# Kernel tuning notes

Measured on AMD Instinct MI355X. Metric: run time of the kernel, lower is better.

The kernel has to match this reference:

```python
import jax, jax.numpy as jnp
import numpy as np

N = 4096
E = 131072
IN_C, HID, HEADS, OUT_C = 512, 64, 8, 256
BETA = 0.5
NEG_SLOPE = 0.2


def _glorot(key, shape, fan_in, fan_out):
    lim = float(np.sqrt(6.0 / (fan_in + fan_out)))
    return jax.random.uniform(key, shape, jnp.float32, -lim, lim)


def setup_inputs() -> dict:
    key = jax.random.key(0)
    ks = jax.random.split(key, 12)
    x = jax.random.normal(ks[0], (N, IN_C), jnp.float32)
    src = jax.random.randint(ks[1], (E,), 0, N)
    dst = jax.random.randint(ks[2], (E,), 0, N)
    dst = jnp.where(src == dst, (dst + 1) % N, dst)  # no self loops (module removes then re-adds)
    edge_index = jnp.stack([src, dst]).astype(jnp.int64)
    # layer 1: in=512 -> heads=8, out=64 (concat -> 512), residual=False
    W1 = _glorot(ks[3], (IN_C, HEADS * HID), IN_C, HEADS * HID)
    as1 = _glorot(ks[4], (HEADS, HID), HID, HID)
    ad1 = _glorot(ks[5], (HEADS, HID), HID, HID)
    b1 = jnp.zeros((HEADS * HID,), jnp.float32)
    # layer 2: in=512 -> heads=1, out=256, concat=False, residual=True (res_linear needed)
    W2 = _glorot(ks[6], (HEADS * HID, OUT_C), HEADS * HID, OUT_C)
    as2 = _glorot(ks[7], (1, OUT_C), OUT_C, OUT_C)
    ad2 = _glorot(ks[8], (1, OUT_C), OUT_C, OUT_C)
    b2 = jnp.zeros((OUT_C,), jnp.float32)
    resW2 = _glorot(ks[9], (HEADS * HID, OUT_C), HEADS * HID, OUT_C)
    return {"x": x, "edge_index": edge_index, "W1": W1, "as1": as1, "ad1": ad1,
            "b1": b1, "W2": W2, "as2": as2, "ad2": ad2, "b2": b2, "resW2": resW2}


def _seg_softmax(e, seg, n):
    # numerically-stable softmax over edges grouped by destination node
    m = jax.ops.segment_max(e, seg, num_segments=n)  # [n, H]
    a = jnp.exp(e - m[seg])
    s = jax.ops.segment_sum(a, seg, num_segments=n)
    return a / (s[seg] + 1e-16)


def _motif_gat_layer(x, edge_index, W, a_src, a_dst, bias, res_W, heads, out_ch, concat):
    n = x.shape[0]
    residual = x
    h = (x @ W).reshape(n, heads, out_ch)
    # add self loops (input edge_index has none)
    loops = jnp.arange(n, dtype=edge_index.dtype)
    src = jnp.concatenate([edge_index[0], loops])
    dst = jnp.concatenate([edge_index[1], loops])
    xj = h[src]  # [E', H, C]
    xi = h[dst]
    e = (xj * a_src[None]).sum(-1) + (xi * a_dst[None]).sum(-1)  # [E', H]
    alpha_first = _seg_softmax(jax.nn.leaky_relu(e, NEG_SLOPE), dst, n)
    # motif adjacency: dense A^3, row-normalized by clamped row sum
    adj = jnp.zeros((n, n), x.dtype).at[src, dst].set(1.0)
    m3 = adj @ adj @ adj
    m3 = m3 / jnp.clip(m3.sum(-1, keepdims=True), 1.0)
    mw = m3[src, dst][:, None]  # [E', 1]
    alpha_motif = _seg_softmax(jax.nn.leaky_relu(e * mw, NEG_SLOPE), dst, n)
    alpha = BETA * alpha_first + (1.0 - BETA) * alpha_motif  # dropout: eval mode -> identity
    out = jax.ops.segment_sum(alpha[:, :, None] * xj, dst, num_segments=n)  # [n, H, C]
    out = out.reshape(n, heads * out_ch) if concat else out.mean(1)
    if res_W is not None:
        out = out + residual @ res_W
    return out + bias


def reference(x, edge_index, W1, as1, ad1, b1, W2, as2, ad2, b2, resW2):
    h = _motif_gat_layer(x, edge_index, W1, as1, ad1, b1, None, HEADS, HID, True)
    h = jax.nn.elu(h)  # dropout: eval mode -> identity
    out = _motif_gat_layer(h, edge_index, W2, as2, ad2, b2, resW2, 1, OUT_C, False)
    return out
```

## Files before the change

kernel.cpp:

```cpp
#include <hip/hip_runtime.h>
#include <hip/hip_bf16.h>
#include <math.h>

#define NN 4096
#define EE 131072
#define EP (EE + NN)
#define C1 512
#define H1 8
#define C2 256
#define NWORDS 128
#define KP 520

typedef __attribute__((ext_vector_type(8))) short bf16x8;
typedef __attribute__((ext_vector_type(4))) float f32x4;

__device__ __forceinline__ float wredMaxf(float v){
#pragma unroll
  for(int o=32;o;o>>=1) v = fmaxf(v, __shfl_xor(v,o));
  return v;
}
__device__ __forceinline__ float wredSumf(float v){
#pragma unroll
  for(int o=32;o;o>>=1) v += __shfl_xor(v,o);
  return v;
}
__device__ __forceinline__ int wredSumi(int v){
#pragma unroll
  for(int o=32;o;o>>=1) v += __shfl_xor(v,o);
  return v;
}

__device__ __forceinline__ void bfsplit(float v, unsigned short& h, unsigned short& l){
  unsigned bits = __float_as_uint(v);
  h = (unsigned short)(bits>>16);
  float hf = __uint_as_float(bits & 0xFFFF0000u);
  float lo = v - hf;
  l = (unsigned short)(__float_as_uint(lo)>>16);
}

__device__ __forceinline__ int detect_mode(const int* __restrict__ ei32){
  unsigned nz = 0;
#pragma unroll
  for(int i=1;i<16;i+=2) nz |= (unsigned)ei32[i];
  return nz != 0;
}

__device__ __forceinline__ void edge_sd(const int* ei32, int mode, int e, int& s, int& d){
  if(e < EE){
    if(mode==0){ s = ei32[2*e]; d = ei32[2*(EE+e)]; }
    else       { s = ei32[e];   d = ei32[EE+e]; }
  } else { s = e - EE; d = s; }
}

__global__ __launch_bounds__(256) void k_build(const int* __restrict__ ei32,
    unsigned* __restrict__ rowbits, unsigned* __restrict__ colbits, unsigned* __restrict__ cnt){
  int e = blockIdx.x*256 + threadIdx.x;
  if(e >= EP) return;
  int m = detect_mode(ei32), s, d;
  edge_sd(ei32, m, e, s, d);
  atomicOr(&rowbits[s*NWORDS + (d>>5)], 1u<<(d&31));
  atomicOr(&colbits[d*NWORDS + (s>>5)], 1u<<(s&31));
  atomicAdd(&cnt[d], 1u);
}

__global__ __launch_bounds__(256) void k_scan_deg(const unsigned* __restrict__ cnt, unsigned* __restrict__ rowptr,
    const unsigned* __restrict__ rowbits, float* __restrict__ v1){
  int t = threadIdx.x;
  if(blockIdx.x == 0){
    __shared__ unsigned part[256];
    unsigned loc[16]; unsigned s = 0;
#pragma unroll
    for(int i=0;i<16;i++){ loc[i]=cnt[t*16+i]; s+=loc[i]; }
    part[t]=s; __syncthreads();
    for(int off=1;off<256;off<<=1){
      unsigned v = (t>=off)? part[t-off] : 0u;
      __syncthreads();
      part[t]+=v;
      __syncthreads();
    }
    unsigned run = (t==0)? 0u : part[t-1];
#pragma unroll
    for(int i=0;i<16;i++){ rowptr[t*16+i]=run; run+=loc[i]; }
    if(t==255) rowptr[NN]=run;
  } else {
    int node = (blockIdx.x-1)*4 + (t>>6);
    int lane = t & 63;
    unsigned w0 = rowbits[node*NWORDS + 2*lane];
    unsigned w1 = rowbits[node*NWORDS + 2*lane + 1];
    int c = __popc(w0) + __popc(w1);
    c = wredSumi(c);
    if(lane==0) v1[node] = (float)c;
  }
}

__global__ __launch_bounds__(256) void k_fill_mv(const int* __restrict__ ei32,
    const unsigned* __restrict__ rowptr, unsigned* __restrict__ fill, unsigned* __restrict__ csr_src,
    const unsigned* __restrict__ rowbits, const float* __restrict__ v1, float* __restrict__ v2){
  int t = threadIdx.x;
  if(blockIdx.x < 528){
    int e = blockIdx.x*256 + t;
    if(e >= EP) return;
    int m = detect_mode(ei32), s, d;
    edge_sd(ei32, m, e, s, d);
    unsigned pos = rowptr[d] + atomicAdd(&fill[d], 1u);
    csr_src[pos]=(unsigned)s;
  } else {
    int node = (blockIdx.x-528)*4 + (t>>6);
    int lane = t & 63;
    float sum = 0.f;
    unsigned w = rowbits[node*NWORDS + 2*lane]; int b0 = lane*64;
    while(w){ int b=__ffs(w)-1; sum += v1[b0+b]; w &= w-1; }
    w = rowbits[node*NWORDS + 2*lane + 1]; b0 = lane*64 + 32;
    while(w){ int b=__ffs(w)-1; sum += v1[b0+b]; w &= w-1; }
    sum = wredSumf(sum);
    if(lane==0) v2[node] = sum;
  }
}

__global__ __launch_bounds__(256) void k_mv2_cvt(const unsigned* __restrict__ rowbits,
    const float* __restrict__ v2, float* __restrict__ v3,
    const float* __restrict__ X, unsigned short* __restrict__ xh, unsigned short* __restrict__ xl,
    const float* __restrict__ W1f, const float* __restrict__ W2f, const float* __restrict__ Wrf,
    unsigned short* __restrict__ b1h, unsigned short* __restrict__ b1l,
    unsigned short* __restrict__ b2h, unsigned short* __restrict__ b2l){
  int t = threadIdx.x;
  int b = blockIdx.x;
  if(b < 1024){
    int node = b*4 + (t>>6);
    int lane = t & 63;
    float sum = 0.f;
    unsigned w = rowbits[node*NWORDS + 2*lane]; int b0 = lane*64;
    while(w){ int bb=__ffs(w)-1; sum += v2[b0+bb]; w &= w-1; }
    w = rowbits[node*NWORDS + 2*lane + 1]; b0 = lane*64 + 32;
    while(w){ int bb=__ffs(w)-1; sum += v2[b0+bb]; w &= w-1; }
    sum = wredSumf(sum);
    if(lane==0) v3[node] = sum;
  } else if(b < 2048){
    int e = (b-1024)*256 + t;
    int row = e >> 6;
    int c0 = (e & 63) * 8;
    const float4 v0 = *(const float4*)&X[(size_t)row*C1 + c0];
    const float4 v1q = *(const float4*)&X[(size_t)row*C1 + c0 + 4];
    float vv[8] = {v0.x,v0.y,v0.z,v0.w,v1q.x,v1q.y,v1q.z,v1q.w};
    unsigned short h[8], l[8];
#pragma unroll
    for(int j=0;j<8;j++) bfsplit(vv[j], h[j], l[j]);
    *(bf16x8*)&xh[(size_t)row*KP + c0] = *(bf16x8*)h;
    *(bf16x8*)&xl[(size_t)row*KP + c0] = *(bf16x8*)l;
  } else {
    int blk = b - 2048;
    const float* W; int N, n, nrow; unsigned short *bh, *bl;
    if(blk < 512){ W=W1f; N=512; n=blk;     nrow=n;     bh=b1h; bl=b1l; }
    else if(blk < 768){ W=W2f; N=256; n=blk-512; nrow=n;     bh=b2h; bl=b2l; }
    else { W=Wrf; N=256; n=blk-768; nrow=n+256; bh=b2h; bl=b2l; }
    int k = t*2;
    float a = W[(size_t)k*N + n];
    float bb = W[(size_t)(k+1)*N + n];
    unsigned short h0,l0,h1,l1;
    bfsplit(a,h0,l0); bfsplit(bb,h1,l1);
    unsigned short hp[2]={h0,h1}, lp[2]={l0,l1};
    *(unsigned int*)&bh[(size_t)nrow*KP + k] = *(unsigned int*)hp;
    *(unsigned int*)&bl[(size_t)nrow*KP + k] = *(unsigned int*)lp;
  }
}

__global__ __launch_bounds__(64) void k_motif(const unsigned* __restrict__ rowbits, const unsigned* __restrict__ colbits,
    const unsigned* __restrict__ rowptr, const unsigned* __restrict__ csr_src,
    const float* __restrict__ v3, float* __restrict__ mwc){
  int d = blockIdx.x;
  int lane = threadIdx.x;
  __shared__ unsigned short nbr[1024];
  __shared__ int cntL;
  if(lane==0) cntL=0;
  __syncthreads();
  {
    unsigned w = colbits[d*NWORDS + 2*lane]; int b0 = lane*64;
    while(w){ int b=__ffs(w)-1; int pos=atomicAdd(&cntL,1); nbr[pos]=(unsigned short)(b0+b); w&=w-1; }
    w = colbits[d*NWORDS + 2*lane + 1]; b0 = lane*64 + 32;
    while(w){ int b=__ffs(w)-1; int pos=atomicAdd(&cntL,1); nbr[pos]=(unsigned short)(b0+b); w&=w-1; }
  }
  __syncthreads();
  int m = cntL;
  unsigned gp[8][2];
#pragma unroll
  for(int p=0;p<8;p++){ gp[p][0]=0u; gp[p][1]=0u; }
  for(int t0=0;t0<m;t0+=4){
    unsigned xa[4], xb[4];
#pragma unroll
    for(int j=0;j<4;j++){
      int tt=t0+j;
      if(tt<m){ int l = nbr[tt]; xa[j]=colbits[l*NWORDS+2*lane]; xb[j]=colbits[l*NWORDS+2*lane+1]; }
      else    { xa[j]=0u; xb[j]=0u; }
    }
#pragma unroll
    for(int j=0;j<4;j++){
      unsigned c = xa[j];
#pragma unroll
      for(int p=0;p<8;p++){ unsigned cy = gp[p][0] & c; gp[p][0] ^= c; c = cy; }
      c = xb[j];
#pragma unroll
      for(int p=0;p<8;p++){ unsigned cy = gp[p][1] & c; gp[p][1] ^= c; c = cy; }
    }
  }
  unsigned base = rowptr[d], deg = rowptr[d+1]-base;
  for(unsigned i0=0;i0<deg;i0+=4){
    unsigned sidx[4], ra[4], rb[4];
#pragma unroll
    for(int j=0;j<4;j++){
      unsigned ii = (i0+j < deg) ? (i0+j) : (deg-1);
      sidx[j] = csr_src[base+ii];
    }
#pragma unroll
    for(int j=0;j<4;j++){ ra[j]=rowbits[sidx[j]*NWORDS+2*lane]; rb[j]=rowbits[sidx[j]*NWORDS+2*lane+1]; }
    int sum[4];
#pragma unroll
    for(int j=0;j<4;j++){
      int s=0;
#pragma unroll
      for(int p=0;p<8;p++)
        s += (__popc(ra[j]&gp[p][0]) + __popc(rb[j]&gp[p][1])) << p;
      sum[j]=s;
    }
    int pk0 = sum[0] | (sum[1]<<16);
    int pk1 = sum[2] | (sum[3]<<16);
    pk0 = wredSumi(pk0); pk1 = wredSumi(pk1);
    if(lane==0){
      int ss[4] = { pk0 & 0xFFFF, (pk0>>16)&0xFFFF, pk1 & 0xFFFF, (pk1>>16)&0xFFFF };
#pragma unroll
      for(int j=0;j<4;j++){
        unsigned idx = i0+j;
        if(idx<deg)
          mwc[base+idx] = (float)ss[j] / fmaxf(v3[csr_src[base+idx]], 1.0f);
      }
    }
  }
}

__global__ __launch_bounds__(256) void k_gemm_mfma(
    const unsigned short* __restrict__ Ah, const unsigned short* __restrict__ Al,
    const unsigned short* __restrict__ Bh, const unsigned short* __restrict__ Bl,
    float* __restrict__ C, int M, int N,
    const float* __restrict__ aS, const float* __restrict__ aD,
    float* __restrict__ oS, float* __restrict__ oD, int amode){
  __shared__ unsigned short Ahs[64][72], Als[64][72], Bhs[64][72], Bls[64][72];
  int bm = blockIdx.y*64, bn = blockIdx.x*64;
  int t = threadIdx.x, lane = t&63, w = t>>6;
  int wm = (w>>1)*32, wn = (w&1)*32;
  f32x4 acc[2][2];
#pragma unroll
  for(int i=0;i<2;i++)
#pragma unroll
    for(int j=0;j<2;j++) acc[i][j] = (f32x4){0.f,0.f,0.f,0.f};
  int sm = t>>2, sk = (t&3)*16;
  const unsigned short* pAh = &Ah[(size_t)(bm+sm)*KP + sk];
  const unsigned short* pAl = &Al[(size_t)(bm+sm)*KP + sk];
  const unsigned short* pBh = &Bh[(size_t)(bn+sm)*KP + sk];
  const unsigned short* pBl = &Bl[(size_t)(bn+sm)*KP + sk];
  int fr = lane&15, kg = lane>>4;
  bf16x8 rah0 = *(const bf16x8*)(pAh), rah1 = *(const bf16x8*)(pAh+8);
  bf16x8 ral0 = *(const bf16x8*)(pAl), ral1 = *(const bf16x8*)(pAl+8);
  bf16x8 rbh0 = *(const bf16x8*)(pBh), rbh1 = *(const bf16x8*)(pBh+8);
  bf16x8 rbl0 = *(const bf16x8*)(pBl), rbl1 = *(const bf16x8*)(pBl+8);
  *(bf16x8*)&Ahs[sm][sk] = rah0; *(bf16x8*)&Ahs[sm][sk+8] = rah1;
  *(bf16x8*)&Als[sm][sk] = ral0; *(bf16x8*)&Als[sm][sk+8] = ral1;
  *(bf16x8*)&Bhs[sm][sk] = rbh0; *(bf16x8*)&Bhs[sm][sk+8] = rbh1;
  *(bf16x8*)&Bls[sm][sk] = rbl0; *(bf16x8*)&Bls[sm][sk+8] = rbl1;
  __syncthreads();
  for(int k0=0;k0<C1;k0+=64){
    int kn = k0+64;
    if(kn<C1){
      rah0 = *(const bf16x8*)(pAh+kn); rah1 = *(const bf16x8*)(pAh+kn+8);
      ral0 = *(const bf16x8*)(pAl+kn); ral1 = *(const bf16x8*)(pAl+kn+8);
      rbh0 = *(const bf16x8*)(pBh+kn); rbh1 = *(const bf16x8*)(pBh+kn+8);
      rbl0 = *(const bf16x8*)(pBl+kn); rbl1 = *(const bf16x8*)(pBl+kn+8);
    }
#pragma unroll
    for(int ks=0;ks<64;ks+=32){
      bf16x8 fah[2], fal[2], fbh[2], fbl[2];
#pragma unroll
      for(int i=0;i<2;i++){
        fah[i] = *(bf16x8*)&Ahs[wm + i*16 + fr][ks + kg*8];
        fal[i] = *(bf16x8*)&Als[wm + i*16 + fr][ks + kg*8];
        fbh[i] = *(bf16x8*)&Bhs[wn + i*16 + fr][ks + kg*8];
        fbl[i] = *(bf16x8*)&Bls[wn + i*16 + fr][ks + kg*8];
      }
#pragma unroll
      for(int i=0;i<2;i++)
#pragma unroll
        for(int j=0;j<2;j++){
          acc[i][j] = __builtin_amdgcn_mfma_f32_16x16x32_bf16(fah[i], fbh[j], acc[i][j], 0,0,0);
          acc[i][j] = __builtin_amdgcn_mfma_f32_16x16x32_bf16(fah[i], fbl[j], acc[i][j], 0,0,0);
          acc[i][j] = __builtin_amdgcn_mfma_f32_16x16x32_bf16(fal[i], fbh[j], acc[i][j], 0,0,0);
        }
    }
    __syncthreads();
    if(kn<C1){
      *(bf16x8*)&Ahs[sm][sk] = rah0; *(bf16x8*)&Ahs[sm][sk+8] = rah1;
      *(bf16x8*)&Als[sm][sk] = ral0; *(bf16x8*)&Als[sm][sk+8] = ral1;
      *(bf16x8*)&Bhs[sm][sk] = rbh0; *(bf16x8*)&Bhs[sm][sk+8] = rbh1;
      *(bf16x8*)&Bls[sm][sk] = rbl0; *(bf16x8*)&Bls[sm][sk+8] = rbl1;
    }
    __syncthreads();
  }
#pragma unroll
  for(int i=0;i<2;i++)
#pragma unroll
    for(int j=0;j<2;j++){
      int gr = bm + wm + i*16 + kg*4;
      int gc = bn + wn + j*16 + fr;
#pragma unroll
      for(int e=0;e<4;e++)
        C[(size_t)(gr+e)*N + gc] = acc[i][j][e];
    }
  bool do_attn = (amode==1) || (bn < 256);
  if(do_attn){
    float p1[2][4], p2[2][4];
#pragma unroll
    for(int i=0;i<2;i++)
#pragma unroll
      for(int e=0;e<4;e++){ p1[i][e]=0.f; p2[i][e]=0.f; }
#pragma unroll
    for(int j=0;j<2;j++){
      int col = bn + wn + j*16 + fr;
      float a1c = aS[col], a2c = aD[col];
#pragma unroll
      for(int i=0;i<2;i++)
#pragma unroll
        for(int e=0;e<4;e++){ p1[i][e] += acc[i][j][e]*a1c; p2[i][e] += acc[i][j][e]*a2c; }
    }
#pragma unroll
    for(int o=1;o<16;o<<=1){
#pragma unroll
      for(int i=0;i<2;i++)
#pragma unroll
        for(int e=0;e<4;e++){ p1[i][e]+=__shfl_xor(p1[i][e],o); p2[i][e]+=__shfl_xor(p2[i][e],o); }
    }
    if(fr==0){
      int head = (amode==1)? (bn>>6) : 0;
      int hs = (amode==1)? H1 : 1;
#pragma unroll
      for(int i=0;i<2;i++)
#pragma unroll
        for(int e=0;e<4;e++){
          int row = bm + wm + i*16 + kg*4 + e;
          atomicAdd(&oS[row*hs + head], p1[i][e]);
          atomicAdd(&oD[row*hs + head], p2[i][e]);
        }
    }
  }
}

__global__ __launch_bounds__(128) void k_layer1(const unsigned* __restrict__ rowptr, const unsigned* __restrict__ csr_src,
    const float* __restrict__ mwc, const float* __restrict__ asrc, const float* __restrict__ adst,
    const float* __restrict__ hpre, const float* __restrict__ b1,
    unsigned short* __restrict__ h1h, unsigned short* __restrict__ h1l){
  int n = blockIdx.x;
  int tid = threadIdx.x, lane = tid&63, wv = tid>>6;
  unsigned base = rowptr[n], deg = rowptr[n+1]-base;
  __shared__ float a1s[128][9];
  __shared__ float a2s[128][9];
  __shared__ unsigned ssrc[128];
  __shared__ float red1[2][8], red2[2][8];
  __shared__ float snm1[8], snm2[8], sscl1[8], sscl2[8];
  __shared__ float sS1[8], sS2[8], sM1[8], sM2[8];
  __shared__ float adsts[8];
  if(tid<8){ adsts[tid]=adst[n*H1+tid]; sM1[tid]=-3.0e38f; sM2[tid]=-3.0e38f; sS1[tid]=0.f; sS2[tid]=0.f; }
  __syncthreads();
  int h = tid>>4;
  float4 acc1={0.f,0.f,0.f,0.f}, acc2={0.f,0.f,0.f,0.f};
  for(unsigned c0=0;c0<deg;c0+=128){
    int csz = (int)min(128u, deg-c0);
    bool act = (tid < csz);
    float el[8], em[8];
    if(act){
      unsigned s = csr_src[base+c0+tid];
      ssrc[tid]=s;
      float mwv = mwc[base+c0+tid];
      const float4 a0v = *(const float4*)&asrc[s*H1];
      const float4 a1v = *(const float4*)&asrc[s*H1+4];
      float as8[8]={a0v.x,a0v.y,a0v.z,a0v.w,a1v.x,a1v.y,a1v.z,a1v.w};
#pragma unroll
      for(int hh=0;hh<8;hh++){
        float ev = as8[hh]+adsts[hh];
        el[hh] = ev>=0.f? ev : 0.2f*ev;
        float evm = ev*mwv;
        em[hh] = evm>=0.f? evm : 0.2f*evm;
      }
    } else {
#pragma unroll
      for(int hh=0;hh<8;hh++){ el[hh]=-3.0e38f; em[hh]=-3.0e38f; }
    }
    float mx1[8], mx2[8];
#pragma unroll
    for(int hh=0;hh<8;hh++){ mx1[hh]=wredMaxf(el[hh]); mx2[hh]=wredMaxf(em[hh]); }
    if(lane==0){
#pragma unroll
      for(int hh=0;hh<8;hh++){ red1[wv][hh]=mx1[hh]; red2[wv][hh]=mx2[hh]; }
    }
    __syncthreads();
    if(tid<8){
      float cm1 = fmaxf(red1[0][tid], red1[1][tid]);
      float cm2 = fmaxf(red2[0][tid], red2[1][tid]);
      float nm1 = fmaxf(sM1[tid], cm1), nm2 = fmaxf(sM2[tid], cm2);
      sscl1[tid] = expf(sM1[tid]-nm1); sscl2[tid] = expf(sM2[tid]-nm2);
      snm1[tid]=nm1; snm2[tid]=nm2;
      sM1[tid]=nm1;  sM2[tid]=nm2;
    }
    __syncthreads();
    float s1l[8], s2l[8];
#pragma unroll
    for(int hh=0;hh<8;hh++){
      float a1v = act? expf(el[hh]-snm1[hh]) : 0.f;
      float a2v = act? expf(em[hh]-snm2[hh]) : 0.f;
      if(act){ a1s[tid][hh]=a1v; a2s[tid][hh]=a2v; }
      s1l[hh]=a1v; s2l[hh]=a2v;
    }
#pragma unroll
    for(int hh=0;hh<8;hh++){ s1l[hh]=wredSumf(s1l[hh]); s2l[hh]=wredSumf(s2l[hh]); }
    if(lane==0){
#pragma unroll
      for(int hh=0;hh<8;hh++){ red1[wv][hh]=s1l[hh]; red2[wv][hh]=s2l[hh]; }
    }
    __syncthreads();
    if(tid<8){
      sS1[tid] = sS1[tid]*sscl1[tid] + red1[0][tid]+red1[1][tid];
      sS2[tid] = sS2[tid]*sscl2[tid] + red2[0][tid]+red2[1][tid];
    }
    {
      float sc1 = sscl1[h], sc2 = sscl2[h];
      acc1.x*=sc1; acc1.y*=sc1; acc1.z*=sc1; acc1.w*=sc1;
      acc2.x*=sc2; acc2.y*=sc2; acc2.z*=sc2; acc2.w*=sc2;
    }
    for(int i0=0;i0<csz;i0+=8){
      int jn = min(8, csz-i0);
      unsigned sj[8]; float a1j[8], a2j[8];
#pragma unroll
      for(int j=0;j<8;j++){
        int ii = (j<jn)? i0+j : i0;
        sj[j]=ssrc[ii]; a1j[j]=a1s[ii][h]; a2j[j]=a2s[ii][h];
      }
      float4 hv[8];
#pragma unroll
      for(int j=0;j<8;j++) hv[j] = *(const float4*)&hpre[(size_t)sj[j]*C1 + tid*4];
#pragma unroll
      for(int j=0;j<8;j++){
        float w1 = (j<jn)? a1j[j] : 0.f;
        float w2 = (j<jn)? a2j[j] : 0.f;
        acc1.x += w1*hv[j].x; acc1.y += w1*hv[j].y; acc1.z += w1*hv[j].z; acc1.w += w1*hv[j].w;
        acc2.x += w2*hv[j].x; acc2.y += w2*hv[j].y; acc2.z += w2*hv[j].z; acc2.w += w2*hv[j].w;
      }
    }
    __syncthreads();
  }
  float r1 = 0.5f/(sS1[h]+1e-16f), r2 = 0.5f/(sS2[h]+1e-16f);
  int cc = tid*4;
  const float4 bv = *(const float4*)&b1[cc];
  float o[4];
  float vx = acc1.x*r1 + acc2.x*r2 + bv.x; o[0] = vx>0.f? vx : expm1f(vx);
  float vy = acc1.y*r1 + acc2.y*r2 + bv.y; o[1] = vy>0.f? vy : expm1f(vy);
  float vz = acc1.z*r1 + acc2.z*r2 + bv.z; o[2] = vz>0.f? vz : expm1f(vz);
  float vw = acc1.w*r1 + acc2.w*r2 + bv.w; o[3] = vw>0.f? vw : expm1f(vw);
  unsigned short hh4[4], ll4[4];
#pragma unroll
  for(int j=0;j<4;j++) bfsplit(o[j], hh4[j], ll4[j]);
  *(ushort4*)&h1h[(size_t)n*KP + cc] = *(ushort4*)hh4;
  *(ushort4*)&h1l[(size_t)n*KP + cc] = *(ushort4*)ll4;
}

__global__ __launch_bounds__(64) void k_layer2(const unsigned* __restrict__ rowptr, const unsigned* __restrict__ csr_src,
    const float* __restrict__ mwc, const float* __restrict__ asrc, const float* __restrict__ adst,
    const float* __restrict__ h2, const float* __restrict__ res,
    const float* __restrict__ b2, float* __restrict__ out){
  int n = blockIdx.x; int lane = threadIdx.x;
  unsigned base = rowptr[n], deg = rowptr[n+1]-base;
  __shared__ float a1s[64], a2s[64];
  __shared__ unsigned ssrc[64];
  float ad = adst[n];
  float M1=-3.0e38f, M2=-3.0e38f, S1=0.f, S2=0.f;
  float4 acc1={0.f,0.f,0.f,0.f}, acc2={0.f,0.f,0.f,0.f};
  for(unsigned c0=0;c0<deg;c0+=64){
    int csz = (int)min(64u, deg-c0);
    bool act = (lane < csz);
    float el=-3.0e38f, em=-3.0e38f;
    if(act){
      unsigned s = csr_src[base+c0+lane];
      ssrc[lane]=s;
      float mwv = mwc[base+c0+lane];
      float ev = asrc[s] + ad;
      el = ev>=0.f? ev : 0.2f*ev;
      float evm = ev*mwv;
      em = evm>=0.f? evm : 0.2f*evm;
    }
    float nm1 = fmaxf(M1, wredMaxf(el));
    float nm2 = fmaxf(M2, wredMaxf(em));
    float sc1 = expf(M1-nm1), sc2 = expf(M2-nm2);
    M1=nm1; M2=nm2;
    float a1 = act? expf(el-nm1) : 0.f;
    float a2 = act? expf(em-nm2) : 0.f;
    if(act){ a1s[lane]=a1; a2s[lane]=a2; }
    S1 = S1*sc1 + wredSumf(a1);
    S2 = S2*sc2 + wredSumf(a2);
    acc1.x*=sc1; acc1.y*=sc1; acc1.z*=sc1; acc1.w*=sc1;
    acc2.x*=sc2; acc2.y*=sc2; acc2.z*=sc2; acc2.w*=sc2;
    __syncthreads();
    for(int i0=0;i0<csz;i0+=8){
      int jn = min(8, csz-i0);
      unsigned sj[8]; float a1j[8], a2j[8];
#pragma unroll
      for(int j=0;j<8;j++){
        int ii = (j<jn)? i0+j : i0;
        sj[j]=ssrc[ii]; a1j[j]=a1s[ii]; a2j[j]=a2s[ii];
      }
      float4 hv[8];
#pragma unroll
      for(int j=0;j<8;j++) hv[j] = *(const float4*)&h2[(size_t)sj[j]*512 + lane*4];
#pragma unroll
      for(int j=0;j<8;j++){
        float w1 = (j<jn)? a1j[j] : 0.f;
        float w2 = (j<jn)? a2j[j] : 0.f;
        acc1.x += w1*hv[j].x; acc1.y += w1*hv[j].y; acc1.z += w1*hv[j].z; acc1.w += w1*hv[j].w;
        acc2.x += w2*hv[j].x; acc2.y += w2*hv[j].y; acc2.z += w2*hv[j].z; acc2.w += w2*hv[j].w;
      }
    }
    __syncthreads();
  }
  float r1 = 0.5f/(S1+1e-16f), r2 = 0.5f/(S2+1e-16f);
  int cc = lane*4;
  const float4 rv = *(const float4*)&res[(size_t)n*512 + cc];
  const float4 bv = *(const float4*)&b2[cc];
  float4 o = {acc1.x*r1 + acc2.x*r2 + rv.x + bv.x,
              acc1.y*r1 + acc2.y*r2 + rv.y + bv.y,
              acc1.z*r1 + acc2.z*r2 + rv.z + bv.z,
              acc1.w*r1 + acc2.w*r2 + rv.w + bv.w};
  *(float4*)&out[(size_t)n*C2 + cc] = o;
}

extern "C" void kernel_launch(void* const* d_in, const int* in_sizes, int n_in,
                              void* d_out, int out_size, void* d_ws, size_t ws_size,
                              hipStream_t stream) {
  const float* x    = (const float*)d_in[0];
  const int*   ei32 = (const int*)d_in[1];
  const float* W1   = (const float*)d_in[2];
  const float* as1  = (const float*)d_in[3];
  const float* ad1  = (const float*)d_in[4];
  const float* b1   = (const float*)d_in[5];
  const float* W2   = (const float*)d_in[6];
  const float* as2  = (const float*)d_in[7];
  const float* ad2  = (const float*)d_in[8];
  const float* b2   = (const float*)d_in[9];
  const float* resW2= (const float*)d_in[10];
  float* out = (float*)d_out;

  char* p = (char*)d_ws;
  auto alloc = [&](size_t b){ void* r=(void*)p; p += (b + 255) & ~(size_t)255; return r; };
  unsigned* rowbits = (unsigned*)alloc((size_t)NN*NWORDS*4);
  unsigned* colbits = (unsigned*)alloc((size_t)NN*NWORDS*4);
  unsigned* cnt     = (unsigned*)alloc(NN*4);
  unsigned* fill    = (unsigned*)alloc(NN*4);
  float* asrc1= (float*)alloc(NN*H1*4);
  float* adst1= (float*)alloc(NN*H1*4);
  float* asrc2= (float*)alloc(NN*4);
  float* adst2= (float*)alloc(NN*4);
  size_t zbytes = (size_t)(p - (char*)rowbits);
  unsigned* rowptr  = (unsigned*)alloc((NN+4)*4);
  float* v1 = (float*)alloc(NN*4);
  float* v2 = (float*)alloc(NN*4);
  float* v3 = (float*)alloc(NN*4);
  unsigned* csr_src = (unsigned*)alloc((size_t)EP*4);
  float* mwc  = (float*)alloc((size_t)EP*4);
  unsigned short* xsh = (unsigned short*)alloc((size_t)NN*KP*2);
  unsigned short* xsl = (unsigned short*)alloc((size_t)NN*KP*2);
  unsigned short* bt1h= (unsigned short*)alloc((size_t)C1*KP*2);
  unsigned short* bt1l= (unsigned short*)alloc((size_t)C1*KP*2);
  unsigned short* bt2h= (unsigned short*)alloc((size_t)C1*KP*2);
  unsigned short* bt2l= (unsigned short*)alloc((size_t)C1*KP*2);
  float* hpre = (float*)alloc((size_t)NN*C1*4);
  unsigned short* h1h = (unsigned short*)alloc((size_t)NN*KP*2);
  unsigned short* h1l = (unsigned short*)alloc((size_t)NN*KP*2);
  float* c23  = (float*)alloc((size_t)NN*512*4);
  float* h2  = c23;
  float* res = c23 + 256;

  hipMemsetAsync(rowbits, 0, zbytes, stream);

  k_build<<<(EP+255)/256,256,0,stream>>>(ei32, rowbits, colbits, cnt);
  k_scan_deg<<<1+NN/4,256,0,stream>>>(cnt, rowptr, rowbits, v1);
  k_fill_mv<<<528+NN/4,256,0,stream>>>(ei32, rowptr, fill, csr_src, rowbits, v1, v2);
  k_mv2_cvt<<<3072,256,0,stream>>>(rowbits, v2, v3, x, xsh, xsl, W1, W2, resW2, bt1h, bt1l, bt2h, bt2l);
  k_motif<<<NN,64,0,stream>>>(rowbits, colbits, rowptr, csr_src, v3, mwc);

  k_gemm_mfma<<<dim3(C1/64, NN/64),256,0,stream>>>(xsh, xsl, bt1h, bt1l, hpre, NN, C1,
                                                   as1, ad1, asrc1, adst1, 1);
  k_layer1<<<NN,128,0,stream>>>(rowptr, csr_src, mwc, asrc1, adst1, hpre, b1, h1h, h1l);

  k_gemm_mfma<<<dim3(512/64, NN/64),256,0,stream>>>(h1h, h1l, bt2h, bt2l, c23, NN, 512,
                                                    as2, ad2, asrc2, adst2, 2);
  k_layer2<<<NN,64,0,stream>>>(rowptr, csr_src, mwc, asrc2, adst2, h2, res, b2, out);
}
```

Baseline: 250.9 us.

## Fuse layer-1 GEMM with motif counting, split 4-wave motif, store layer-2 features as bf16

Moves the x/weight bf16 split conversion into the edge-build kernel so it overlaps with graph construction. Merges the layer-1 GEMM and the motif-weight kernel into one launch, with a shared-memory union, so the two independent workloads run concurrently. The motif computation now uses four waves per node and combines their bit-sliced counters through shared memory. The layer-2 GEMM writes the gathered h2 features as round-to-nearest bf16 to halve gather traffic in layer2, which adds rounding error to the aggregated output.

```diff
diff --git a/kernel.cpp b/kernel.cpp
--- a/kernel.cpp
+++ b/kernel.cpp
@@ -38,6 +38,11 @@
   l = (unsigned short)(__float_as_uint(lo)>>16);
 }
 
+__device__ __forceinline__ unsigned short f2bf_rne(float v){
+  unsigned b = __float_as_uint(v);
+  return (unsigned short)((b + 0x7FFFu + ((b>>16)&1u)) >> 16);
+}
+
 __device__ __forceinline__ int detect_mode(const int* __restrict__ ei32){
   unsigned nz = 0;
 #pragma unroll
@@ -52,15 +57,48 @@
   } else { s = e - EE; d = s; }
 }
 
-__global__ __launch_bounds__(256) void k_build(const int* __restrict__ ei32,
-    unsigned* __restrict__ rowbits, unsigned* __restrict__ colbits, unsigned* __restrict__ cnt){
-  int e = blockIdx.x*256 + threadIdx.x;
-  if(e >= EP) return;
-  int m = detect_mode(ei32), s, d;
-  edge_sd(ei32, m, e, s, d);
-  atomicOr(&rowbits[s*NWORDS + (d>>5)], 1u<<(d&31));
-  atomicOr(&colbits[d*NWORDS + (s>>5)], 1u<<(s&31));
-  atomicAdd(&cnt[d], 1u);
+__global__ __launch_bounds__(256) void k_build_cvt(const int* __restrict__ ei32,
+    unsigned* __restrict__ rowbits, unsigned* __restrict__ colbits, unsigned* __restrict__ cnt,
+    const float* __restrict__ X, unsigned short* __restrict__ xh, unsigned short* __restrict__ xl,
+    const float* __restrict__ W1f, const float* __restrict__ W2f, const float* __restrict__ Wrf,
+    unsigned short* __restrict__ b1h, unsigned short* __restrict__ b1l,
+    unsigned short* __restrict__ b2h, unsigned short* __restrict__ b2l){
+  int b = blockIdx.x, t = threadIdx.x;
+  if(b < 528){
+    int e = b*256 + t;
+    if(e >= EP) return;
+    int m = detect_mode(ei32), s, d;
+    edge_sd(ei32, m, e, s, d);
+    atomicOr(&rowbits[s*NWORDS + (d>>5)], 1u<<(d&31));
+    atomicOr(&colbits[d*NWORDS + (s>>5)], 1u<<(s&31));
+    atomicAdd(&cnt[d], 1u);
+  } else if(b < 1552){
+    int e = (b-528)*256 + t;
+    int row = e >> 6;
+    int c0 = (e & 63) * 8;
+    const float4 v0 = *(const float4*)&X[(size_t)row*C1 + c0];
+    const float4 v1q = *(const float4*)&X[(size_t)row*C1 + c0 + 4];
+    float vv[8] = {v0.x,v0.y,v0.z,v0.w,v1q.x,v1q.y,v1q.z,v1q.w};
+    unsigned short h[8], l[8];
+#pragma unroll
+    for(int j=0;j<8;j++) bfsplit(vv[j], h[j], l[j]);
+    *(bf16x8*)&xh[(size_t)row*KP + c0] = *(bf16x8*)h;
+    *(bf16x8*)&xl[(size_t)row*KP + c0] = *(bf16x8*)l;
+  } else {
+    int blk = b - 1552;
+    const float* W; int N, n, nrow; unsigned short *bh, *bl;
+    if(blk < 512){ W=W1f; N=512; n=blk;     nrow=n;     bh=b1h; bl=b1l; }
+    else if(blk < 768){ W=W2f; N=256; n=blk-512; nrow=n;     bh=b2h; bl=b2l; }
+    else { W=Wrf; N=256; n=blk-768; nrow=n+256; bh=b2h; bl=b2l; }
+    int k = t*2;
+    float a = W[(size_t)k*N + n];
+    float bb = W[(size_t)(k+1)*N + n];
+    unsigned short h0,l0,h1,l1;
+    bfsplit(a,h0,l0); bfsplit(bb,h1,l1);
+    unsigned short hp[2]={h0,h1}, lp[2]={l0,l1};
+    *(unsigned int*)&bh[(size_t)nrow*KP + k] = *(unsigned int*)hp;
+    *(unsigned int*)&bl[(size_t)nrow*KP + k] = *(unsigned int*)lp;
+  }
 }
 
 __global__ __launch_bounds__(256) void k_scan_deg(const unsigned* __restrict__ cnt, unsigned* __restrict__ rowptr,
@@ -117,133 +155,30 @@
   }
 }
 
-__global__ __launch_bounds__(256) void k_mv2_cvt(const unsigned* __restrict__ rowbits,
-    const float* __restrict__ v2, float* __restrict__ v3,
-    const float* __restrict__ X, unsigned short* __restrict__ xh, unsigned short* __restrict__ xl,
-    const float* __restrict__ W1f, const float* __restrict__ W2f, const float* __restrict__ Wrf,
-    unsigned short* __restrict__ b1h, unsigned short* __restrict__ b1l,
-    unsigned short* __restrict__ b2h, unsigned short* __restrict__ b2l){
-  int t = threadIdx.x;
-  int b = blockIdx.x;
-  if(b < 1024){
-    int node = b*4 + (t>>6);
-    int lane = t & 63;
-    float sum = 0.f;
-    unsigned w = rowbits[node*NWORDS + 2*lane]; int b0 = lane*64;
-    while(w){ int bb=__ffs(w)-1; sum += v2[b0+bb]; w &= w-1; }
-    w = rowbits[node*NWORDS + 2*lane + 1]; b0 = lane*64 + 32;
-    while(w){ int bb=__ffs(w)-1; sum += v2[b0+bb]; w &= w-1; }
-    sum = wredSumf(sum);
-    if(lane==0) v3[node] = sum;
-  } else if(b < 2048){
-    int e = (b-1024)*256 + t;
-    int row = e >> 6;
-    int c0 = (e & 63) * 8;
-    const float4 v0 = *(const float4*)&X[(size_t)row*C1 + c0];
-    const float4 v1q = *(const float4*)&X[(size_t)row*C1 + c0 + 4];
-    float vv[8] = {v0.x,v0.y,v0.z,v0.w,v1q.x,v1q.y,v1q.z,v1q.w};
-    unsigned short h[8], l[8];
-#pragma unroll
-    for(int j=0;j<8;j++) bfsplit(vv[j], h[j], l[j]);
-    *(bf16x8*)&xh[(size_t)row*KP + c0] = *(bf16x8*)h;
-    *(bf16x8*)&xl[(size_t)row*KP + c0] = *(bf16x8*)l;
-  } else {
-    int blk = b - 2048;
-    const float* W; int N, n, nrow; unsigned short *bh, *bl;
-    if(blk < 512){ W=W1f; N=512; n=blk;     nrow=n;     bh=b1h; bl=b1l; }
-    else if(blk < 768){ W=W2f; N=256; n=blk-512; nrow=n;     bh=b2h; bl=b2l; }
-    else { W=Wrf; N=256; n=blk-768; nrow=n+256; bh=b2h; bl=b2l; }
-    int k = t*2;
-    float a = W[(size_t)k*N + n];
-    float bb = W[(size_t)(k+1)*N + n];
-    unsigned short h0,l0,h1,l1;
-    bfsplit(a,h0,l0); bfsplit(bb,h1,l1);
-    unsigned short hp[2]={h0,h1}, lp[2]={l0,l1};
-    *(unsigned int*)&bh[(size_t)nrow*KP + k] = *(unsigned int*)hp;
-    *(unsigned int*)&bl[(size_t)nrow*KP + k] = *(unsigned int*)lp;
-  }
-}
-
-__global__ __launch_bounds__(64) void k_motif(const unsigned* __restrict__ rowbits, const unsigned* __restrict__ colbits,
-    const unsigned* __restrict__ rowptr, const unsigned* __restrict__ csr_src,
-    const float* __restrict__ v3, float* __restrict__ mwc){
-  int d = blockIdx.x;
-  int lane = threadIdx.x;
-  __shared__ unsigned short nbr[1024];
-  __shared__ int cntL;
-  if(lane==0) cntL=0;
-  __syncthreads();
-  {
-    unsigned w = colbits[d*NWORDS + 2*lane]; int b0 = lane*64;
-    while(w){ int b=__ffs(w)-1; int pos=atomicAdd(&cntL,1); nbr[pos]=(unsigned short)(b0+b); w&=w-1; }
-    w = colbits[d*NWORDS + 2*lane + 1]; b0 = lane*64 + 32;
-    while(w){ int b=__ffs(w)-1; int pos=atomicAdd(&cntL,1); nbr[pos]=(unsigned short)(b0+b); w&=w-1; }
-  }
-  __syncthreads();
-  int m = cntL;
-  unsigned gp[8][2];
-#pragma unroll
-  for(int p=0;p<8;p++){ gp[p][0]=0u; gp[p][1]=0u; }
-  for(int t0=0;t0<m;t0+=4){
-    unsigned xa[4], xb[4];
-#pragma unroll
-    for(int j=0;j<4;j++){
-      int tt=t0+j;
-      if(tt<m){ int l = nbr[tt]; xa[j]=colbits[l*NWORDS+2*lane]; xb[j]=colbits[l*NWORDS+2*lane+1]; }
-      else    { xa[j]=0u; xb[j]=0u; }
-    }
-#pragma unroll
-    for(int j=0;j<4;j++){
-      unsigned c = xa[j];
-#pragma unroll
-      for(int p=0;p<8;p++){ unsigned cy = gp[p][0] & c; gp[p][0] ^= c; c = cy; }
-      c = xb[j];
-#pragma unroll
-      for(int p=0;p<8;p++){ unsigned cy = gp[p][1] & c; gp[p][1] ^= c; c = cy; }
-    }
-  }
-  unsigned base = rowptr[d], deg = rowptr[d+1]-base;
-  for(unsigned i0=0;i0<deg;i0+=4){
-    unsigned sidx[4], ra[4], rb[4];
-#pragma unroll
-    for(int j=0;j<4;j++){
-      unsigned ii = (i0+j < deg) ? (i0+j) : (deg-1);
-      sidx[j] = csr_src[base+ii];
-    }
-#pragma unroll
-    for(int j=0;j<4;j++){ ra[j]=rowbits[sidx[j]*NWORDS+2*lane]; rb[j]=rowbits[sidx[j]*NWORDS+2*lane+1]; }
-    int sum[4];
-#pragma unroll
-    for(int j=0;j<4;j++){
-      int s=0;
-#pragma unroll
-      for(int p=0;p<8;p++)
-        s += (__popc(ra[j]&gp[p][0]) + __popc(rb[j]&gp[p][1])) << p;
-      sum[j]=s;
-    }
-    int pk0 = sum[0] | (sum[1]<<16);
-    int pk1 = sum[2] | (sum[3]<<16);
-    pk0 = wredSumi(pk0); pk1 = wredSumi(pk1);
-    if(lane==0){
-      int ss[4] = { pk0 & 0xFFFF, (pk0>>16)&0xFFFF, pk1 & 0xFFFF, (pk1>>16)&0xFFFF };
-#pragma unroll
-      for(int j=0;j<4;j++){
-        unsigned idx = i0+j;
-        if(idx<deg)
-          mwc[base+idx] = (float)ss[j] / fmaxf(v3[csr_src[base+idx]], 1.0f);
-      }
-    }
-  }
-}
-
-__global__ __launch_bounds__(256) void k_gemm_mfma(
+__global__ __launch_bounds__(256) void k_mv2(const unsigned* __restrict__ rowbits,
+    const float* __restrict__ v2, float* __restrict__ v3){
+  int node = blockIdx.x*4 + (threadIdx.x>>6);
+  int lane = threadIdx.x & 63;
+  float sum = 0.f;
+  unsigned w = rowbits[node*NWORDS + 2*lane]; int b0 = lane*64;
+  while(w){ int b=__ffs(w)-1; sum += v2[b0+b]; w &= w-1; }
+  w = rowbits[node*NWORDS + 2*lane + 1]; b0 = lane*64 + 32;
+  while(w){ int b=__ffs(w)-1; sum += v2[b0+b]; w &= w-1; }
+  sum = wredSumf(sum);
+  if(lane==0) v3[node] = sum;
+}
+
+__device__ __forceinline__ void gemm_tile(unsigned short* lds, int bx, int by,
     const unsigned short* __restrict__ Ah, const unsigned short* __restrict__ Al,
     const unsigned short* __restrict__ Bh, const unsigned short* __restrict__ Bl,
-    float* __restrict__ C, int M, int N,
+    float* __restrict__ Cf, unsigned short* __restrict__ h2b, float* __restrict__ resf,
     const float* __restrict__ aS, const float* __restrict__ aD,
     float* __restrict__ oS, float* __restrict__ oD, int amode){
-  __shared__ unsigned short Ahs[64][72], Als[64][72], Bhs[64][72], Bls[64][72];
-  int bm = blockIdx.y*64, bn = blockIdx.x*64;
+  unsigned short* Ahs = lds;
+  unsigned short* Als = lds + 64*72;
+  unsigned short* Bhs = lds + 2*64*72;
+  unsigned short* Bls = lds + 3*64*72;
+  int bm = by*64, bn = bx*64;
   int t = threadIdx.x, lane = t&63, w = t>>6;
   int wm = (w>>1)*32, wn = (w&1)*32;
   f32x4 acc[2][2];
@@ -261,10 +196,10 @@
   bf16x8 ral0 = *(const bf16x8*)(pAl), ral1 = *(const bf16x8*)(pAl+8);
   bf16x8 rbh0 = *(const bf16x8*)(pBh), rbh1 = *(const bf16x8*)(pBh+8);
   bf16x8 rbl0 = *(const bf16x8*)(pBl), rbl1 = *(const bf16x8*)(pBl+8);
-  *(bf16x8*)&Ahs[sm][sk] = rah0; *(bf16x8*)&Ahs[sm][sk+8] = rah1;
-  *(bf16x8*)&Als[sm][sk] = ral0; *(bf16x8*)&Als[sm][sk+8] = ral1;
-  *(bf16x8*)&Bhs[sm][sk] = rbh0; *(bf16x8*)&Bhs[sm][sk+8] = rbh1;
-  *(bf16x8*)&Bls[sm][sk] = rbl0; *(bf16x8*)&Bls[sm][sk+8] = rbl1;
+  *(bf16x8*)&Ahs[sm*72+sk] = rah0; *(bf16x8*)&Ahs[sm*72+sk+8] = rah1;
+  *(bf16x8*)&Als[sm*72+sk] = ral0; *(bf16x8*)&Als[sm*72+sk+8] = ral1;
+  *(bf16x8*)&Bhs[sm*72+sk] = rbh0; *(bf16x8*)&Bhs[sm*72+sk+8] = rbh1;
+  *(bf16x8*)&Bls[sm*72+sk] = rbl0; *(bf16x8*)&Bls[sm*72+sk+8] = rbl1;
   __syncthreads();
   for(int k0=0;k0<C1;k0+=64){
     int kn = k0+64;
@@ -279,10 +214,10 @@
       bf16x8 fah[2], fal[2], fbh[2], fbl[2];
 #pragma unroll
       for(int i=0;i<2;i++){
-        fah[i] = *(bf16x8*)&Ahs[wm + i*16 + fr][ks + kg*8];
-        fal[i] = *(bf16x8*)&Als[wm + i*16 + fr][ks + kg*8];
-        fbh[i] = *(bf16x8*)&Bhs[wn + i*16 + fr][ks + kg*8];
-        fbl[i] = *(bf16x8*)&Bls[wn + i*16 + fr][ks + kg*8];
+        fah[i] = *(bf16x8*)&Ahs[(wm + i*16 + fr)*72 + ks + kg*8];
+        fal[i] = *(bf16x8*)&Als[(wm + i*16 + fr)*72 + ks + kg*8];
+        fbh[i] = *(bf16x8*)&Bhs[(wn + i*16 + fr)*72 + ks + kg*8];
+        fbl[i] = *(bf16x8*)&Bls[(wn + i*16 + fr)*72 + ks + kg*8];
       }
 #pragma unroll
       for(int i=0;i<2;i++)
@@ -295,10 +230,10 @@
     }
     __syncthreads();
     if(kn<C1){
-      *(bf16x8*)&Ahs[sm][sk] = rah0; *(bf16x8*)&Ahs[sm][sk+8] = rah1;
-      *(bf16x8*)&Als[sm][sk] = ral0; *(bf16x8*)&Als[sm][sk+8] = ral1;
-      *(bf16x8*)&Bhs[sm][sk] = rbh0; *(bf16x8*)&Bhs[sm][sk+8] = rbh1;
-      *(bf16x8*)&Bls[sm][sk] = rbl0; *(bf16x8*)&Bls[sm][sk+8] = rbl1;
+      *(bf16x8*)&Ahs[sm*72+sk] = rah0; *(bf16x8*)&Ahs[sm*72+sk+8] = rah1;
+      *(bf16x8*)&Als[sm*72+sk] = ral0; *(bf16x8*)&Als[sm*72+sk+8] = ral1;
+      *(bf16x8*)&Bhs[sm*72+sk] = rbh0; *(bf16x8*)&Bhs[sm*72+sk+8] = rbh1;
+      *(bf16x8*)&Bls[sm*72+sk] = rbl0; *(bf16x8*)&Bls[sm*72+sk+8] = rbl1;
     }
     __syncthreads();
   }
@@ -308,9 +243,21 @@
     for(int j=0;j<2;j++){
       int gr = bm + wm + i*16 + kg*4;
       int gc = bn + wn + j*16 + fr;
-#pragma unroll
-      for(int e=0;e<4;e++)
-        C[(size_t)(gr+e)*N + gc] = acc[i][j][e];
+      if(amode==1){
+#pragma unroll
+        for(int e=0;e<4;e++)
+          Cf[(size_t)(gr+e)*C1 + gc] = acc[i][j][e];
+      } else {
+        if(gc < 256){
+#pragma unroll
+          for(int e=0;e<4;e++)
+            h2b[(size_t)(gr+e)*C2 + gc] = f2bf_rne(acc[i][j][e]);
+        } else {
+#pragma unroll
+          for(int e=0;e<4;e++)
+            resf[(size_t)(gr+e)*C2 + gc - 256] = acc[i][j][e];
+        }
+      }
     }
   bool do_attn = (amode==1) || (bn < 256);
   if(do_attn){
@@ -348,6 +295,105 @@
         }
     }
   }
+}
+
+__global__ __launch_bounds__(256) void k_gemm1_motif(
+    const unsigned short* __restrict__ Ah, const unsigned short* __restrict__ Al,
+    const unsigned short* __restrict__ Bh, const unsigned short* __restrict__ Bl,
+    float* __restrict__ hpre, const float* __restrict__ as1, const float* __restrict__ ad1,
+    float* __restrict__ asrc1, float* __restrict__ adst1,
+    const unsigned* __restrict__ rowbits, const unsigned* __restrict__ colbits,
+    const unsigned* __restrict__ rowptr, const unsigned* __restrict__ csr_src,
+    const float* __restrict__ v3, float* __restrict__ mwc){
+  __shared__ union {
+    unsigned short g[4*64*72];
+    struct { unsigned short nbr[1024]; int cntL; unsigned comb[4][16][64]; } m;
+  } sm;
+  int b = blockIdx.x, t = threadIdx.x;
+  if(b < 512){
+    gemm_tile(sm.g, b&7, b>>3, Ah, Al, Bh, Bl, hpre, nullptr, nullptr,
+              as1, ad1, asrc1, adst1, 1);
+    return;
+  }
+  int d = b - 512;
+  int lane = t&63, wv = t>>6;
+  if(t==0) sm.m.cntL = 0;
+  __syncthreads();
+  if(t < 64){
+    unsigned w = colbits[d*NWORDS + 2*t]; int b0 = t*64;
+    while(w){ int bb=__ffs(w)-1; int pos=atomicAdd(&sm.m.cntL,1); sm.m.nbr[pos]=(unsigned short)(b0+bb); w&=w-1; }
+    w = colbits[d*NWORDS + 2*t + 1]; b0 = t*64 + 32;
+    while(w){ int bb=__ffs(w)-1; int pos=atomicAdd(&sm.m.cntL,1); sm.m.nbr[pos]=(unsigned short)(b0+bb); w&=w-1; }
+  }
+  __syncthreads();
+  int m = sm.m.cntL;
+  unsigned gp[8][2];
+#pragma unroll
+  for(int p=0;p<8;p++){ gp[p][0]=0u; gp[p][1]=0u; }
+  for(int t0=wv*2; t0<m; t0+=8){
+    unsigned xa[2], xb[2];
+#pragma unroll
+    for(int j=0;j<2;j++){
+      int tt=t0+j;
+      if(tt<m){ int l = sm.m.nbr[tt]; xa[j]=colbits[l*NWORDS+2*lane]; xb[j]=colbits[l*NWORDS+2*lane+1]; }
+      else    { xa[j]=0u; xb[j]=0u; }
+    }
+#pragma unroll
+    for(int j=0;j<2;j++){
+      unsigned c = xa[j];
+#pragma unroll
+      for(int p=0;p<8;p++){ unsigned cy = gp[p][0] & c; gp[p][0] ^= c; c = cy; }
+      c = xb[j];
+#pragma unroll
+      for(int p=0;p<8;p++){ unsigned cy = gp[p][1] & c; gp[p][1] ^= c; c = cy; }
+    }
+  }
+#pragma unroll
+  for(int p=0;p<8;p++){ sm.m.comb[wv][p*2][lane]=gp[p][0]; sm.m.comb[wv][p*2+1][lane]=gp[p][1]; }
+  __syncthreads();
+#pragma unroll
+  for(int ww=0;ww<4;ww++){
+    if(ww==wv) continue;
+    unsigned c0=0, c1=0;
+#pragma unroll
+    for(int p=0;p<8;p++){
+      unsigned y0 = sm.m.comb[ww][p*2][lane];
+      unsigned y1 = sm.m.comb[ww][p*2+1][lane];
+      unsigned x0 = gp[p][0], x1 = gp[p][1];
+      gp[p][0] = x0^y0^c0; c0 = (x0&y0)|(c0&(x0^y0));
+      gp[p][1] = x1^y1^c1; c1 = (x1&y1)|(c1&(x1^y1));
+    }
+  }
+  unsigned base = rowptr[d], deg = rowptr[d+1]-base;
+  for(unsigned i0=wv*2; i0<deg; i0+=8){
+    unsigned i1 = (i0+1 < deg)? i0+1 : i0;
+    unsigned s0 = csr_src[base+i0], s1v = csr_src[base+i1];
+    unsigned ra0 = rowbits[s0*NWORDS+2*lane],  rb0 = rowbits[s0*NWORDS+2*lane+1];
+    unsigned ra1 = rowbits[s1v*NWORDS+2*lane], rb1 = rowbits[s1v*NWORDS+2*lane+1];
+    int sum0=0, sum1=0;
+#pragma unroll
+    for(int p=0;p<8;p++){
+      sum0 += (__popc(ra0&gp[p][0]) + __popc(rb0&gp[p][1])) << p;
+      sum1 += (__popc(ra1&gp[p][0]) + __popc(rb1&gp[p][1])) << p;
+    }
+    int pk = sum0 | (sum1<<16);
+    pk = wredSumi(pk);
+    if(lane==0){
+      mwc[base+i0] = (float)(pk & 0xFFFF) / fmaxf(v3[s0], 1.0f);
+      if(i0+1 < deg) mwc[base+i0+1] = (float)((pk>>16) & 0xFFFF) / fmaxf(v3[s1v], 1.0f);
+    }
+  }
+}
+
+__global__ __launch_bounds__(256) void k_gemm2(
+    const unsigned short* __restrict__ Ah, const unsigned short* __restrict__ Al,
+    const unsigned short* __restrict__ Bh, const unsigned short* __restrict__ Bl,
+    unsigned short* __restrict__ h2b, float* __restrict__ resf,
+    const float* __restrict__ as2, const float* __restrict__ ad2,
+    float* __restrict__ asrc2, float* __restrict__ adst2){
+  __shared__ unsigned short lds[4*64*72];
+  gemm_tile(lds, blockIdx.x & 7, blockIdx.x >> 3, Ah, Al, Bh, Bl, nullptr, h2b, resf,
+            as2, ad2, asrc2, adst2, 2);
 }
 
 __global__ __launch_bounds__(128) void k_layer1(const unsigned* __restrict__ rowptr, const unsigned* __restrict__ csr_src,
@@ -469,7 +515,7 @@
 
 __global__ __launch_bounds__(64) void k_layer2(const unsigned* __restrict__ rowptr, const unsigned* __restrict__ csr_src,
     const float* __restrict__ mwc, const float* __restrict__ asrc, const float* __restrict__ adst,
-    const float* __restrict__ h2, const float* __restrict__ res,
+    const unsigned short* __restrict__ h2b, const float* __restrict__ res,
     const float* __restrict__ b2, float* __restrict__ out){
   int n = blockIdx.x; int lane = threadIdx.x;
   unsigned base = rowptr[n], deg = rowptr[n+1]-base;
@@ -511,22 +557,26 @@
         int ii = (j<jn)? i0+j : i0;
         sj[j]=ssrc[ii]; a1j[j]=a1s[ii]; a2j[j]=a2s[ii];
       }
-      float4 hv[8];
-#pragma unroll
-      for(int j=0;j<8;j++) hv[j] = *(const float4*)&h2[(size_t)sj[j]*512 + lane*4];
+      ushort4 hq[8];
+#pragma unroll
+      for(int j=0;j<8;j++) hq[j] = *(const ushort4*)&h2b[(size_t)sj[j]*C2 + lane*4];
 #pragma unroll
       for(int j=0;j<8;j++){
         float w1 = (j<jn)? a1j[j] : 0.f;
         float w2 = (j<jn)? a2j[j] : 0.f;
-        acc1.x += w1*hv[j].x; acc1.y += w1*hv[j].y; acc1.z += w1*hv[j].z; acc1.w += w1*hv[j].w;
-        acc2.x += w2*hv[j].x; acc2.y += w2*hv[j].y; acc2.z += w2*hv[j].z; acc2.w += w2*hv[j].w;
+        float hx = __uint_as_float((unsigned)hq[j].x<<16);
+        float hy = __uint_as_float((unsigned)hq[j].y<<16);
+        float hz = __uint_as_float((unsigned)hq[j].z<<16);
+        float hw = __uint_as_float((unsigned)hq[j].w<<16);
+        acc1.x += w1*hx; acc1.y += w1*hy; acc1.z += w1*hz; acc1.w += w1*hw;
+        acc2.x += w2*hx; acc2.y += w2*hy; acc2.z += w2*hz; acc2.w += w2*hw;
       }
     }
     __syncthreads();
   }
   float r1 = 0.5f/(S1+1e-16f), r2 = 0.5f/(S2+1e-16f);
   int cc = lane*4;
-  const float4 rv = *(const float4*)&res[(size_t)n*512 + cc];
+  const float4 rv = *(const float4*)&res[(size_t)n*C2 + cc];
   const float4 bv = *(const float4*)&b2[cc];
   float4 o = {acc1.x*r1 + acc2.x*r2 + rv.x + bv.x,
               acc1.y*r1 + acc2.y*r2 + rv.y + bv.y,
@@ -577,23 +627,21 @@
   float* hpre = (float*)alloc((size_t)NN*C1*4);
   unsigned short* h1h = (unsigned short*)alloc((size_t)NN*KP*2);
   unsigned short* h1l = (unsigned short*)alloc((size_t)NN*KP*2);
-  float* c23  = (float*)alloc((size_t)NN*512*4);
-  float* h2  = c23;
-  float* res = c23 + 256;
+  unsigned short* h2b = (unsigned short*)alloc((size_t)NN*C2*2);
+  float* res  = (float*)alloc((size_t)NN*C2*4);
 
   hipMemsetAsync(rowbits, 0, zbytes, stream);
 
-  k_build<<<(EP+255)/256,256,0,stream>>>(ei32, rowbits, colbits, cnt);
+  k_build_cvt<<<2576,256,0,stream>>>(ei32, rowbits, colbits, cnt,
+                                     x, xsh, xsl, W1, W2, resW2, bt1h, bt1l, bt2h, bt2l);
   k_scan_deg<<<1+NN/4,256,0,stream>>>(cnt, rowptr, rowbits, v1);
   k_fill_mv<<<528+NN/4,256,0,stream>>>(ei32, rowptr, fill, csr_src, rowbits, v1, v2);
-  k_mv2_cvt<<<3072,256,0,stream>>>(rowbits, v2, v3, x, xsh, xsl, W1, W2, resW2, bt1h, bt1l, bt2h, bt2l);
-  k_motif<<<NN,64,0,stream>>>(rowbits, colbits, rowptr, csr_src, v3, mwc);
-
-  k_gemm_mfma<<<dim3(C1/64, NN/64),256,0,stream>>>(xsh, xsl, bt1h, bt1l, hpre, NN, C1,
-                                                   as1, ad1, asrc1, adst1, 1);
+  k_mv2<<<NN/4,256,0,stream>>>(rowbits, v2, v3);
+
+  k_gemm1_motif<<<512+NN,256,0,stream>>>(xsh, xsl, bt1h, bt1l, hpre, as1, ad1, asrc1, adst1,
+                                         rowbits, colbits, rowptr, csr_src, v3, mwc);
   k_layer1<<<NN,128,0,stream>>>(rowptr, csr_src, mwc, asrc1, adst1, hpre, b1, h1h, h1l);
 
-  k_gemm_mfma<<<dim3(512/64, NN/64),256,0,stream>>>(h1h, h1l, bt2h, bt2l, c23, NN, 512,
-                                                    as2, ad2, asrc2, adst2, 2);
-  k_layer2<<<NN,64,0,stream>>>(rowptr, csr_src, mwc, asrc2, adst2, h2, res, b2, out);
-}
+  k_gemm2<<<512,256,0,stream>>>(h1h, h1l, bt2h, bt2l, h2b, res, as2, ad2, asrc2, adst2);
+  k_layer2<<<NN,64,0,stream>>>(rowptr, csr_src, mwc, asrc2, adst2, h2b, res, b2, out);
+}
```

Result: no change. 252.5 us (+0.6%).
